# Optimization experiments

Hardware: AMD Instinct MI355X
Metric: run time of the kernel (lower is better)

The kernel has to match this reference:

```python
import jax, jax.numpy as jnp
import numpy as np

EPS = 1e-5  # torch LayerNorm default

def _layer_norm(v, w, b):
    mu = jnp.mean(v, axis=-1, keepdims=True)
    var = jnp.mean(jnp.square(v - mu), axis=-1, keepdims=True)
    return (v - mu) * jax.lax.rsqrt(var + EPS) * w + b

def _gru_layer(x, h0, w_ih, b_ih, w_hh, b_hh, ln_w, ln_b):
    # x: [B,T,in], h0: [B,H]
    H = h0.shape[-1]
    # precompute input gates for whole sequence: [B,T,3H]
    x_gates = jnp.einsum('bti,gi->btg', x, w_ih) + b_ih

    def step(h, xg_t):
        hg = jnp.einsum('bh,gh->bg', h, w_hh) + b_hh
        x_r, x_z, x_n = jnp.split(xg_t, 3, axis=-1)
        h_r, h_z, h_n = jnp.split(hg, 3, axis=-1)
        r = jax.nn.sigmoid(_layer_norm(x_r + h_r, ln_w[0], ln_b[0]))
        z = jax.nn.sigmoid(_layer_norm(x_z + h_z, ln_w[1], ln_b[1]))
        n = jnp.tanh(_layer_norm(x_n + r * h_n, ln_w[2], ln_b[2]))
        h_new = (1 - z) * n + z * h
        return h_new, h_new

    h_final, ys = jax.lax.scan(step, h0, jnp.swapaxes(x_gates, 0, 1))
    return jnp.swapaxes(ys, 0, 1), h_final  # [B,T,H], [B,H]

def setup_inputs() -> dict:
    key = jax.random.key(0)
    ks = jax.random.split(key, 4)
    B, T, D, H, L = 64, 512, 768, 768, 2
    G = 3 * H
    x = jax.random.normal(ks[0], (B, T, D), dtype=jnp.float32)
    h_0 = jnp.zeros((L, B, H), dtype=jnp.float32)
    # scaled gaussian stands in for orthogonal init
    w_ih = jax.random.normal(ks[1], (L, G, D), dtype=jnp.float32) / np.sqrt(D)
    w_hh = jax.random.normal(ks[2], (L, G, H), dtype=jnp.float32) / np.sqrt(H)
    b_ih = jnp.zeros((L, G), dtype=jnp.float32)
    b_hh = jnp.zeros((L, G), dtype=jnp.float32)
    ln_w = jnp.ones((L, 3, H), dtype=jnp.float32)
    ln_b = jnp.zeros((L, 3, H), dtype=jnp.float32)
    return {"x": x, "h_0": h_0, "w_ih": w_ih, "b_ih": b_ih,
            "w_hh": w_hh, "b_hh": b_hh, "ln_w": ln_w, "ln_b": ln_b}

def reference(x, h_0, w_ih, b_ih, w_hh, b_hh, ln_w, ln_b):
    num_layers = h_0.shape[0]
    layer_output = x
    x_residual = x  # input_size == hidden_size -> identity residual
    finals = []
    for i in range(num_layers):
        seq, h_fin = _gru_layer(layer_output, h_0[i], w_ih[i], b_ih[i],
                                w_hh[i], b_hh[i], ln_w[i], ln_b[i])
        if i == 0:
            seq = seq + x_residual
        else:
            seq = seq + layer_output
        layer_output = seq  # dropout=0.0, eval mode -> no-op
        finals.append(h_fin)
    h_final_stack = jnp.stack(finals, axis=0)
    return layer_output, h_final_stack
```

## Files before the change

### kernel.cpp

```cpp
#include <hip/hip_runtime.h>

typedef short bf16x8 __attribute__((ext_vector_type(8)));
typedef float f32x4 __attribute__((ext_vector_type(4)));

__device__ __forceinline__ unsigned pack2bf(float a, float b) {
  union { float f; unsigned u; } x, y;
  x.f = a; y.f = b;
  unsigned ra = (x.u + 0x7FFFu + ((x.u >> 16) & 1u)) >> 16;
  unsigned rb = (y.u + 0x7FFFu + ((y.u >> 16) & 1u)) & 0xFFFF0000u;
  return ra | rb;
}
__device__ __forceinline__ unsigned short bfu(float f) {
  union { float f; unsigned u; } v; v.f = f;
  return (unsigned short)((v.u + 0x7FFFu + ((v.u >> 16) & 1u)) >> 16);
}
__device__ __forceinline__ float sigf(float x) { return 1.f / (1.f + __expf(-x)); }

#define KB 64
#define LDSP 72

__global__ __launch_bounds__(256) void gemm_bt(
    const float* __restrict__ A0, size_t a_bstride,
    const float* __restrict__ W,
    const float* __restrict__ bias,
    float* __restrict__ out, size_t o_bstride,
    int Mvalid)
{
  __shared__ unsigned short As[64][LDSP];
  __shared__ unsigned short Bs[64][LDSP];
  const int tid = threadIdx.x;
  const int g0 = blockIdx.x * 64;
  const float* Ab = A0 + (size_t)blockIdx.y * a_bstride;
  float* outb = out + (size_t)blockIdx.y * o_bstride;

  const int srow = tid >> 2;
  const int scol = (tid & 3) << 4;
  const int wv = tid >> 6;
  const int lane = tid & 63;
  const int wr = wv >> 1, wc = wv & 1;
  const int lrow = lane & 15;
  const int lk = (lane >> 4) << 3;

  f32x4 acc[2][2];
#pragma unroll
  for (int i = 0; i < 2; ++i)
#pragma unroll
    for (int j = 0; j < 2; ++j)
      acc[i][j] = (f32x4){0.f, 0.f, 0.f, 0.f};

  const float* Aptr = Ab + (size_t)srow * 768 + scol;
  const float* Bptr = W + ((size_t)(g0 + srow)) * 768 + scol;
  const bool aval = srow < Mvalid;

  for (int k0 = 0; k0 < 768; k0 += KB) {
    uint4 ua0, ua1, ub0, ub1;
    if (aval) {
      const float4* qa = (const float4*)(Aptr + k0);
      float4 f0 = qa[0], f1 = qa[1], f2 = qa[2], f3 = qa[3];
      ua0 = make_uint4(pack2bf(f0.x, f0.y), pack2bf(f0.z, f0.w),
                       pack2bf(f1.x, f1.y), pack2bf(f1.z, f1.w));
      ua1 = make_uint4(pack2bf(f2.x, f2.y), pack2bf(f2.z, f2.w),
                       pack2bf(f3.x, f3.y), pack2bf(f3.z, f3.w));
    } else {
      ua0 = make_uint4(0u, 0u, 0u, 0u);
      ua1 = ua0;
    }
    {
      const float4* qb = (const float4*)(Bptr + k0);
      float4 f0 = qb[0], f1 = qb[1], f2 = qb[2], f3 = qb[3];
      ub0 = make_uint4(pack2bf(f0.x, f0.y), pack2bf(f0.z, f0.w),
                       pack2bf(f1.x, f1.y), pack2bf(f1.z, f1.w));
      ub1 = make_uint4(pack2bf(f2.x, f2.y), pack2bf(f2.z, f2.w),
                       pack2bf(f3.x, f3.y), pack2bf(f3.z, f3.w));
    }
    __syncthreads();
    *(uint4*)&As[srow][scol] = ua0;
    *(uint4*)&As[srow][scol + 8] = ua1;
    *(uint4*)&Bs[srow][scol] = ub0;
    *(uint4*)&Bs[srow][scol + 8] = ub1;
    __syncthreads();
#pragma unroll
    for (int kh = 0; kh < 2; ++kh) {
      bf16x8 a0 = *(const bf16x8*)&As[32 * wr + lrow][32 * kh + lk];
      bf16x8 a1 = *(const bf16x8*)&As[32 * wr + 16 + lrow][32 * kh + lk];
      bf16x8 b0 = *(const bf16x8*)&Bs[32 * wc + lrow][32 * kh + lk];
      bf16x8 b1 = *(const bf16x8*)&Bs[32 * wc + 16 + lrow][32 * kh + lk];
      acc[0][0] = __builtin_amdgcn_mfma_f32_16x16x32_bf16(a0, b0, acc[0][0], 0, 0, 0);
      acc[0][1] = __builtin_amdgcn_mfma_f32_16x16x32_bf16(a0, b1, acc[0][1], 0, 0, 0);
      acc[1][0] = __builtin_amdgcn_mfma_f32_16x16x32_bf16(a1, b0, acc[1][0], 0, 0, 0);
      acc[1][1] = __builtin_amdgcn_mfma_f32_16x16x32_bf16(a1, b1, acc[1][1], 0, 0, 0);
    }
  }

  const int lgrp = lane >> 4;
#pragma unroll
  for (int fr = 0; fr < 2; ++fr)
#pragma unroll
    for (int fc = 0; fc < 2; ++fc)
#pragma unroll
      for (int j = 0; j < 4; ++j) {
        int m = 32 * wr + 16 * fr + lgrp * 4 + j;
        int n = 32 * wc + 16 * fc + lrow;
        if (m < Mvalid)
          outb[(size_t)m * 2304 + g0 + n] = acc[fr][fc][j] + bias[g0 + n];
      }
}

#define NWG 72
#define EPS 1e-5f
#define INV768 (1.0f / 768.0f)
#define SLOT 24576u

__device__ __forceinline__ void bar_arrive(unsigned* c) {
  __syncthreads();
  if (threadIdx.x == 0)
    __hip_atomic_fetch_add(c + (blockIdx.x & 7) * 32, 1u,
                           __ATOMIC_RELAXED, __HIP_MEMORY_SCOPE_AGENT);
}
__device__ __forceinline__ void bar_wait(unsigned* c, unsigned tgt) {
  if (threadIdx.x == 0) {
    for (;;) {
      unsigned s = 0;
#pragma unroll
      for (int i = 0; i < 8; ++i)
        s += __hip_atomic_load(c + i * 32, __ATOMIC_RELAXED, __HIP_MEMORY_SCOPE_AGENT);
      if (s >= tgt) break;
      __builtin_amdgcn_s_sleep(1);
    }
  }
  __syncthreads();
}

template <int N>
__device__ __forceinline__ void blk_reduce(float* v, float* lds) {
#pragma unroll
  for (int k = 0; k < N; ++k) {
    float x = v[k];
#pragma unroll
    for (int off = 1; off < 64; off <<= 1) x += __shfl_xor(x, off);
    v[k] = x;
  }
  const int wv = threadIdx.x >> 6;
  const int lane = threadIdx.x & 63;
  if (lane == 0) {
#pragma unroll
    for (int k = 0; k < N; ++k) lds[wv * N + k] = v[k];
  }
  __syncthreads();
#pragma unroll
  for (int k = 0; k < N; ++k)
    v[k] = lds[k] + lds[N + k] + lds[2 * N + k] + lds[3 * N + k];
  __syncthreads();
}

#define WAITV(n) do { asm volatile("s_waitcnt vmcnt(" #n ")" ::: "memory"); \
                      __builtin_amdgcn_sched_barrier(0); } while (0)

#define LD24(buf, base) \
  { _Pragma("unroll") for (int kk_ = 0; kk_ < 24; ++kk_) { \
      const unsigned* p_ = (base) + (size_t)kk_ * 1024u; \
      asm volatile("global_load_dwordx4 %0, %1, off sc0 sc1" : "=v"(buf[kk_]) : "v"(p_)); } }

#define WRRING(ring, t, val) \
  { unsigned* rp_ = (ring) + (unsigned)(((t) & 3)) * SLOT; \
    _Pragma("unroll") for (int p_ = 0; p_ < 3; ++p_) { \
      int i_ = tid + (p_ << 8); \
      float other_ = __shfl_xor(val[p_], 1); \
      if ((tid & 1) == 0) { \
        unsigned pk_ = pack2bf(val[p_], other_); \
        __hip_atomic_store(rp_ + (i_ >> 3) * 256 + b * 4 + ((i_ >> 1) & 3), pk_, \
                           __ATOMIC_RELAXED, __HIP_MEMORY_SCOPE_AGENT); } } }

__global__ __launch_bounds__(256, 1) void gru_super(
    const float* __restrict__ Whh1, const float* __restrict__ bhh1,
    const float* __restrict__ Wih2, const float* __restrict__ bih2,
    const float* __restrict__ Whh2, const float* __restrict__ bhh2,
    const float* __restrict__ lnw, const float* __restrict__ lnb,
    const float* __restrict__ x,
    const float* __restrict__ xg1,
    int t0, int TC,
    const float* __restrict__ h0,
    float* __restrict__ hstate,
    unsigned* __restrict__ h1ring, unsigned* __restrict__ s1ring,
    unsigned* __restrict__ h2ring,
    float* __restrict__ hg1, float* __restrict__ xg2, float* __restrict__ hg2,
    unsigned* __restrict__ bar,
    float* __restrict__ seq,
    float* __restrict__ hfin,
    int firstflag, int lastflag)
{
  __shared__ unsigned short Wl[96][776];
  __shared__ float bl96[96];
  __shared__ float redl[32];

  unsigned* barA = bar;
  unsigned* barB = bar + 512;

  const int wg = blockIdx.x;
  const int tid = threadIdx.x;
  const int lane = tid & 63;
  const int w = tid >> 6;
  const int la = lane & 15;
  const int kb = lane >> 4;
  const int arow = 16 * w + la;
  const int mcls = wg / 24;
  const int g0w = (wg % 24) * 96;
  const unsigned abase = (unsigned)((kb * 64 + arow) << 2);

  {
    const float* Wsrc = (mcls == 0) ? Whh1 : (mcls == 1) ? Wih2 : Whh2;
    const float* bsrc = (mcls == 0) ? bhh1 : (mcls == 1) ? bih2 : bhh2;
    for (int r = 0; r < 96; ++r) {
      const float* src = Wsrc + (size_t)(g0w + r) * 768;
      for (int c = tid; c < 768; c += 256) Wl[r][c] = bfu(src[c]);
    }
    if (tid < 96) bl96[tid] = bsrc[g0w + tid];
  }
  float* dst = (mcls == 0) ? hg1 : (mcls == 1) ? xg2 : hg2;

  const int b = wg;
  float hreg1[3] = {0.f,0.f,0.f}, hreg2[3] = {0.f,0.f,0.f};
  float h1prev[3] = {0.f,0.f,0.f}, xprev[3] = {0.f,0.f,0.f}, xcur[3] = {0.f,0.f,0.f};
  float lw1[9], lb1[9], lw2[9], lb2[9];
  if (wg < 64) {
#pragma unroll
    for (int g = 0; g < 3; ++g)
#pragma unroll
      for (int p = 0; p < 3; ++p) {
        int idx = g * 3 + p, gi = g * 768 + tid + (p << 8);
        lw1[idx] = lnw[gi];          lb1[idx] = lnb[gi];
        lw2[idx] = lnw[2304 + gi];   lb2[idx] = lnb[2304 + gi];
      }
#pragma unroll
    for (int p = 0; p < 3; ++p) {
      int i = tid + (p << 8);
      hreg1[p] = firstflag ? h0[(size_t)b * 768 + i] : hstate[(size_t)b * 768 + i];
      hreg2[p] = firstflag ? h0[49152 + (size_t)b * 768 + i] : hstate[49152 + (size_t)b * 768 + i];
      h1prev[p] = hreg1[p];
    }
    if (firstflag) {
      WRRING(h1ring, 3, hreg1);
      WRRING(h2ring, 3, hreg2);
    }
  }
  bar_arrive(barB);
  bar_wait(barB, NWG);

  for (int s = 0; s <= TC; ++s) {
    const int t1 = t0 + s;
    const bool doL1 = (s < TC);
    const bool doL2 = (s >= 1);
    const bool active = (mcls == 0) ? doL1 : doL2;

    if (active) {
      const unsigned* rbase =
          (mcls == 0) ? (h1ring + (unsigned)((t1 - 1) & 3) * SLOT)
        : (mcls == 1) ? (s1ring + (unsigned)((t1 - 1) & 3) * SLOT)
                      : (h2ring + (unsigned)((t1 - 2) & 3) * SLOT);
      const unsigned* hb = rbase + abase;
      f32x4 acc[6];
#pragma unroll
      for (int r = 0; r < 6; ++r) acc[r] = (f32x4){0.f, 0.f, 0.f, 0.f};
      bf16x8 buf[24];
      LD24(buf, hb);
      WAITV(0);
#pragma unroll
      for (int kk = 0; kk < 24; ++kk) {
#pragma unroll
        for (int r = 0; r < 6; ++r) {
          bf16x8 wv = *(const bf16x8*)&Wl[16 * r + la][kk * 32 + kb * 8];
          acc[r] = __builtin_amdgcn_mfma_f32_16x16x32_bf16(buf[kk], wv, acc[r], 0, 0, 0);
        }
      }
#pragma unroll
      for (int r = 0; r < 6; ++r)
#pragma unroll
        for (int j = 0; j < 4; ++j) {
          int bb = 16 * w + kb * 4 + j;
          __hip_atomic_store(dst + (size_t)bb * 2304 + g0w + 16 * r + la,
                             acc[r][j] + bl96[16 * r + la],
                             __ATOMIC_RELAXED, __HIP_MEMORY_SCOPE_AGENT);
        }
    }

    if (wg < 64 && doL1) {
#pragma unroll
      for (int p = 0; p < 3; ++p)
        xcur[p] = x[((size_t)b * 512 + t1) * 768 + tid + (p << 8)];
    }

    bar_arrive(barA);
    bar_wait(barA, (unsigned)(s + 1) * NWG);

    if (wg < 64) {
      const int ttc = doL1 ? s : (TC - 1);
      float g1v[9], g2v[9], g3v[9], x1v[9];
      {
        const float* xg1b = xg1 + ((size_t)b * TC + ttc) * 2304;
        const float* p1 = hg1 + (size_t)b * 2304;
        const float* p2 = xg2 + (size_t)b * 2304;
        const float* p3 = hg2 + (size_t)b * 2304;
#pragma unroll
        for (int p = 0; p < 9; ++p) {
          x1v[p] = xg1b[tid + p * 256];
          const float* q1 = p1 + tid + p * 256;
          const float* q2 = p2 + tid + p * 256;
          const float* q3 = p3 + tid + p * 256;
          asm volatile("global_load_dword %0, %1, off sc0 sc1" : "=v"(g1v[p]) : "v"(q1));
          asm volatile("global_load_dword %0, %1, off sc0 sc1" : "=v"(g2v[p]) : "v"(q2));
          asm volatile("global_load_dword %0, %1, off sc0 sc1" : "=v"(g3v[p]) : "v"(q3));
        }
      }
      WAITV(0);

      float s11[3], s21[3], s12[3], s22[3];
      float v8[8] = {0,0,0,0,0,0,0,0};
#pragma unroll
      for (int p = 0; p < 3; ++p) {
        s11[p] = g1v[p] + x1v[p];
        s21[p] = g1v[3 + p] + x1v[3 + p];
        s12[p] = g2v[p] + g3v[p];
        s22[p] = g2v[3 + p] + g3v[3 + p];
        v8[0] += s11[p]; v8[1] += s11[p] * s11[p];
        v8[2] += s21[p]; v8[3] += s21[p] * s21[p];
        v8[4] += s12[p]; v8[5] += s12[p] * s12[p];
        v8[6] += s22[p]; v8[7] += s22[p] * s22[p];
      }
      blk_reduce<8>(v8, redl);
      float mu11 = v8[0] * INV768, rs11 = rsqrtf(v8[1] * INV768 - mu11 * mu11 + EPS);
      float mu21 = v8[2] * INV768, rs21 = rsqrtf(v8[3] * INV768 - mu21 * mu21 + EPS);
      float mu12 = v8[4] * INV768, rs12 = rsqrtf(v8[5] * INV768 - mu12 * mu12 + EPS);
      float mu22 = v8[6] * INV768, rs22 = rsqrtf(v8[7] * INV768 - mu22 * mu22 + EPS);

      float z1[3], m1[3], z2[3], m2[3];
      float v4[4] = {0,0,0,0};
#pragma unroll
      for (int p = 0; p < 3; ++p) {
        float r1 = sigf((s11[p] - mu11) * rs11 * lw1[p] + lb1[p]);
        z1[p]    = sigf((s21[p] - mu21) * rs21 * lw1[3 + p] + lb1[3 + p]);
        m1[p] = x1v[6 + p] + r1 * g1v[6 + p];
        float r2 = sigf((s12[p] - mu12) * rs12 * lw2[p] + lb2[p]);
        z2[p]    = sigf((s22[p] - mu22) * rs22 * lw2[3 + p] + lb2[3 + p]);
        m2[p] = g2v[6 + p] + r2 * g3v[6 + p];
        v4[0] += m1[p]; v4[1] += m1[p] * m1[p];
        v4[2] += m2[p]; v4[3] += m2[p] * m2[p];
      }
      blk_reduce<4>(v4, redl);
      float mum1 = v4[0] * INV768, rsm1 = rsqrtf(v4[1] * INV768 - mum1 * mum1 + EPS);
      float mum2 = v4[2] * INV768, rsm2 = rsqrtf(v4[3] * INV768 - mum2 * mum2 + EPS);

      float h1new[3], s1new[3], h2new[3];
#pragma unroll
      for (int p = 0; p < 3; ++p) {
        float n1 = tanhf((m1[p] - mum1) * rsm1 * lw1[6 + p] + lb1[6 + p]);
        h1new[p] = (1.f - z1[p]) * n1 + z1[p] * hreg1[p];
        s1new[p] = h1new[p] + xcur[p];
        float n2 = tanhf((m2[p] - mum2) * rsm2 * lw2[6 + p] + lb2[6 + p]);
        h2new[p] = (1.f - z2[p]) * n2 + z2[p] * hreg2[p];
      }
      if (doL2) {
        const int t2 = t1 - 1;
#pragma unroll
        for (int p = 0; p < 3; ++p) {
          int i = tid + (p << 8);
          hreg2[p] = h2new[p];
          seq[((size_t)b * 512 + t2) * 768 + i] = h2new[p] + h1prev[p] + xprev[p];
        }
        WRRING(h2ring, t1 - 1, h2new);
      }
      if (doL1) {
#pragma unroll
        for (int p = 0; p < 3; ++p) {
          hreg1[p] = h1new[p];
          h1prev[p] = h1new[p];
          xprev[p] = xcur[p];
        }
        WRRING(h1ring, t1, h1new);
        WRRING(s1ring, t1, s1new);
      }
    }
    bar_arrive(barB);
    bar_wait(barB, (unsigned)(s + 2) * NWG);
  }

  if (wg < 64) {
#pragma unroll
    for (int p = 0; p < 3; ++p) {
      int i = tid + (p << 8);
      hstate[(size_t)b * 768 + i] = hreg1[p];
      hstate[49152 + (size_t)b * 768 + i] = hreg2[p];
      if (lastflag) {
        hfin[(size_t)b * 768 + i] = hreg1[p];
        hfin[49152 + (size_t)b * 768 + i] = hreg2[p];
      }
    }
  }
}

extern "C" void kernel_launch(void* const* d_in, const int* in_sizes, int n_in,
                              void* d_out, int out_size, void* d_ws, size_t ws_size,
                              hipStream_t stream) {
  const float* x    = (const float*)d_in[0];
  const float* h0   = (const float*)d_in[1];
  const float* w_ih = (const float*)d_in[2];
  const float* b_ih = (const float*)d_in[3];
  const float* w_hh = (const float*)d_in[4];
  const float* b_hh = (const float*)d_in[5];
  const float* lnw  = (const float*)d_in[6];
  const float* lnb  = (const float*)d_in[7];
  float* out = (float*)d_out;

  const int B = 64, T = 512, H = 768, G = 2304;

  const size_t BAR = 65536;
  const size_t RING = 4u * SLOT * 4u;
  const size_t HGB = (size_t)B * G * 4;
  int CHUNK = 64;
  for (;;) {
    size_t need = BAR + 3 * RING + 3 * HGB + 2 * (size_t)B * H * 4
                + (size_t)B * CHUNK * G * 4;
    if (need <= ws_size || CHUNK == 8) break;
    CHUNK >>= 1;
  }

  char* wp = (char*)d_ws;
  unsigned* barctr = (unsigned*)wp;            wp += BAR;
  unsigned* h1ring = (unsigned*)wp;            wp += RING;
  unsigned* s1ring = (unsigned*)wp;            wp += RING;
  unsigned* h2ring = (unsigned*)wp;            wp += RING;
  float* hg1 = (float*)wp;                     wp += HGB;
  float* xg2 = (float*)wp;                     wp += HGB;
  float* hg2 = (float*)wp;                     wp += HGB;
  float* hstate = (float*)wp;                  wp += 2 * (size_t)B * H * 4;
  float* xg1 = (float*)wp;

  hipMemsetAsync(barctr, 0, BAR, stream);

  float* seq  = out;
  float* hfin = out + (size_t)B * T * H;
  const int NCH = T / CHUNK;

  const float* Wih1 = w_ih;
  const float* Wih2 = w_ih + (size_t)G * H;
  const float* Whh1 = w_hh;
  const float* Whh2 = w_hh + (size_t)G * H;

  for (int c = 0; c < NCH; ++c) {
    int t0 = c * CHUNK;
    gemm_bt<<<dim3(G / 64, B), 256, 0, stream>>>(
        x + (size_t)t0 * H, (size_t)T * H, Wih1, b_ih,
        xg1, (size_t)CHUNK * G, CHUNK);
    gru_super<<<NWG, 256, 0, stream>>>(
        Whh1, b_hh, Wih2, b_ih + G, Whh2, b_hh + G,
        lnw, lnb, x, xg1, t0, CHUNK,
        h0, hstate, h1ring, s1ring, h2ring,
        hg1, xg2, hg2,
        barctr + (size_t)c * 1024,
        seq, hfin,
        (c == 0) ? 1 : 0, (c == NCH - 1) ? 1 : 0);
  }
}
```

Measured before the change: 7.532 ms.

## Split GRU persistent kernel into producer matmul and consumer gate workgroups

The persistent recurrent kernel now uses 72 producer workgroups that only do the hidden-state matmuls and 64 separate consumer workgroups that do the LayerNorm/gate math. A symmetric full barrier per step is replaced by one-directional producer/consumer counters, so each side waits only on the other. Consumers prefetch xg1 and x before waiting and defer the seq store until after signalling. The chunk size doubles to 128 with a z-dimension added to the input GEMM to cover the extra rows. This is meant to cut barrier latency and overlap the two phases, at the cost of more resident workgroups (136) and a larger xg1 workspace.

```diff
diff --git a/kernel.cpp b/kernel.cpp
--- a/kernel.cpp
+++ b/kernel.cpp
@@ -30,8 +30,9 @@
   __shared__ unsigned short Bs[64][LDSP];
   const int tid = threadIdx.x;
   const int g0 = blockIdx.x * 64;
-  const float* Ab = A0 + (size_t)blockIdx.y * a_bstride;
-  float* outb = out + (size_t)blockIdx.y * o_bstride;
+  const int mlo = blockIdx.z * 64;
+  const float* Ab = A0 + (size_t)blockIdx.y * a_bstride + (size_t)mlo * 768;
+  float* outb = out + (size_t)blockIdx.y * o_bstride + (size_t)mlo * 2304;
 
   const int srow = tid >> 2;
   const int scol = (tid & 3) << 4;
@@ -50,7 +51,7 @@
 
   const float* Aptr = Ab + (size_t)srow * 768 + scol;
   const float* Bptr = W + ((size_t)(g0 + srow)) * 768 + scol;
-  const bool aval = srow < Mvalid;
+  const bool aval = (mlo + srow) < Mvalid;
 
   for (int k0 = 0; k0 < 768; k0 += KB) {
     uint4 ua0, ua1, ub0, ub1;
@@ -101,12 +102,14 @@
       for (int j = 0; j < 4; ++j) {
         int m = 32 * wr + 16 * fr + lgrp * 4 + j;
         int n = 32 * wc + 16 * fc + lrow;
-        if (m < Mvalid)
+        if (mlo + m < Mvalid)
           outb[(size_t)m * 2304 + g0 + n] = acc[fr][fc][j] + bias[g0 + n];
       }
 }
 
-#define NWG 72
+#define NWGP 72
+#define NWGC 64
+#define NWGT 136
 #define EPS 1e-5f
 #define INV768 (1.0f / 768.0f)
 #define SLOT 24576u
@@ -203,196 +206,205 @@
   const int la = lane & 15;
   const int kb = lane >> 4;
   const int arow = 16 * w + la;
-  const int mcls = wg / 24;
-  const int g0w = (wg % 24) * 96;
-  const unsigned abase = (unsigned)((kb * 64 + arow) << 2);
-
-  {
-    const float* Wsrc = (mcls == 0) ? Whh1 : (mcls == 1) ? Wih2 : Whh2;
-    const float* bsrc = (mcls == 0) ? bhh1 : (mcls == 1) ? bih2 : bhh2;
-    for (int r = 0; r < 96; ++r) {
-      const float* src = Wsrc + (size_t)(g0w + r) * 768;
-      for (int c = tid; c < 768; c += 256) Wl[r][c] = bfu(src[c]);
-    }
-    if (tid < 96) bl96[tid] = bsrc[g0w + tid];
-  }
-  float* dst = (mcls == 0) ? hg1 : (mcls == 1) ? xg2 : hg2;
-
-  const int b = wg;
-  float hreg1[3] = {0.f,0.f,0.f}, hreg2[3] = {0.f,0.f,0.f};
-  float h1prev[3] = {0.f,0.f,0.f}, xprev[3] = {0.f,0.f,0.f}, xcur[3] = {0.f,0.f,0.f};
+
+  if (wg < NWGP) {
+    const int mcls = wg / 24;
+    const int g0w = (wg % 24) * 96;
+    const unsigned abase = (unsigned)((kb * 64 + arow) << 2);
+    {
+      const float* Wsrc = (mcls == 0) ? Whh1 : (mcls == 1) ? Wih2 : Whh2;
+      const float* bsrc = (mcls == 0) ? bhh1 : (mcls == 1) ? bih2 : bhh2;
+      for (int r = 0; r < 96; ++r) {
+        const float* src = Wsrc + (size_t)(g0w + r) * 768;
+        for (int c = tid; c < 768; c += 256) Wl[r][c] = bfu(src[c]);
+      }
+      if (tid < 96) bl96[tid] = bsrc[g0w + tid];
+    }
+    float* dst = (mcls == 0) ? hg1 : (mcls == 1) ? xg2 : hg2;
+
+    for (int s = 0; s <= TC; ++s) {
+      const int t1 = t0 + s;
+      const bool active = (mcls == 0) ? (s < TC) : (s >= 1);
+      bar_wait(barB, 64u * (unsigned)(s + 1));
+      if (active) {
+        const unsigned* rbase =
+            (mcls == 0) ? (h1ring + (unsigned)((t1 - 1) & 3) * SLOT)
+          : (mcls == 1) ? (s1ring + (unsigned)((t1 - 1) & 3) * SLOT)
+                        : (h2ring + (unsigned)((t1 - 2) & 3) * SLOT);
+        const unsigned* hb = rbase + abase;
+        f32x4 acc[6];
+#pragma unroll
+        for (int r = 0; r < 6; ++r) acc[r] = (f32x4){0.f, 0.f, 0.f, 0.f};
+        bf16x8 buf[24];
+        LD24(buf, hb);
+        WAITV(0);
+#pragma unroll
+        for (int kk = 0; kk < 24; ++kk) {
+#pragma unroll
+          for (int r = 0; r < 6; ++r) {
+            bf16x8 wv2 = *(const bf16x8*)&Wl[16 * r + la][kk * 32 + kb * 8];
+            acc[r] = __builtin_amdgcn_mfma_f32_16x16x32_bf16(buf[kk], wv2, acc[r], 0, 0, 0);
+          }
+        }
+#pragma unroll
+        for (int r = 0; r < 6; ++r)
+#pragma unroll
+          for (int j = 0; j < 4; ++j) {
+            int bb = 16 * w + kb * 4 + j;
+            __hip_atomic_store(dst + (size_t)bb * 2304 + g0w + 16 * r + la,
+                               acc[r][j] + bl96[16 * r + la],
+                               __ATOMIC_RELAXED, __HIP_MEMORY_SCOPE_AGENT);
+          }
+      }
+      bar_arrive(barA);
+    }
+    return;
+  }
+
+  const int b = wg - NWGP;
+  float hreg1[3], hreg2[3];
+  float h1prev[3], xprev[3] = {0.f, 0.f, 0.f}, xcur[3] = {0.f, 0.f, 0.f};
   float lw1[9], lb1[9], lw2[9], lb2[9];
-  if (wg < 64) {
-#pragma unroll
-    for (int g = 0; g < 3; ++g)
-#pragma unroll
-      for (int p = 0; p < 3; ++p) {
-        int idx = g * 3 + p, gi = g * 768 + tid + (p << 8);
-        lw1[idx] = lnw[gi];          lb1[idx] = lnb[gi];
-        lw2[idx] = lnw[2304 + gi];   lb2[idx] = lnb[2304 + gi];
-      }
+#pragma unroll
+  for (int g = 0; g < 3; ++g)
 #pragma unroll
     for (int p = 0; p < 3; ++p) {
-      int i = tid + (p << 8);
-      hreg1[p] = firstflag ? h0[(size_t)b * 768 + i] : hstate[(size_t)b * 768 + i];
-      hreg2[p] = firstflag ? h0[49152 + (size_t)b * 768 + i] : hstate[49152 + (size_t)b * 768 + i];
-      h1prev[p] = hreg1[p];
-    }
-    if (firstflag) {
-      WRRING(h1ring, 3, hreg1);
-      WRRING(h2ring, 3, hreg2);
-    }
+      int idx = g * 3 + p, gi = g * 768 + tid + (p << 8);
+      lw1[idx] = lnw[gi];          lb1[idx] = lnb[gi];
+      lw2[idx] = lnw[2304 + gi];   lb2[idx] = lnb[2304 + gi];
+    }
+#pragma unroll
+  for (int p = 0; p < 3; ++p) {
+    int i = tid + (p << 8);
+    hreg1[p] = firstflag ? h0[(size_t)b * 768 + i] : hstate[(size_t)b * 768 + i];
+    hreg2[p] = firstflag ? h0[49152 + (size_t)b * 768 + i] : hstate[49152 + (size_t)b * 768 + i];
+    h1prev[p] = hreg1[p];
+  }
+  if (firstflag) {
+    WRRING(h1ring, 3, hreg1);
+    WRRING(h2ring, 3, hreg2);
   }
   bar_arrive(barB);
-  bar_wait(barB, NWG);
 
   for (int s = 0; s <= TC; ++s) {
     const int t1 = t0 + s;
     const bool doL1 = (s < TC);
     const bool doL2 = (s >= 1);
-    const bool active = (mcls == 0) ? doL1 : doL2;
-
-    if (active) {
-      const unsigned* rbase =
-          (mcls == 0) ? (h1ring + (unsigned)((t1 - 1) & 3) * SLOT)
-        : (mcls == 1) ? (s1ring + (unsigned)((t1 - 1) & 3) * SLOT)
-                      : (h2ring + (unsigned)((t1 - 2) & 3) * SLOT);
-      const unsigned* hb = rbase + abase;
-      f32x4 acc[6];
-#pragma unroll
-      for (int r = 0; r < 6; ++r) acc[r] = (f32x4){0.f, 0.f, 0.f, 0.f};
-      bf16x8 buf[24];
-      LD24(buf, hb);
-      WAITV(0);
-#pragma unroll
-      for (int kk = 0; kk < 24; ++kk) {
-#pragma unroll
-        for (int r = 0; r < 6; ++r) {
-          bf16x8 wv = *(const bf16x8*)&Wl[16 * r + la][kk * 32 + kb * 8];
-          acc[r] = __builtin_amdgcn_mfma_f32_16x16x32_bf16(buf[kk], wv, acc[r], 0, 0, 0);
-        }
-      }
-#pragma unroll
-      for (int r = 0; r < 6; ++r)
-#pragma unroll
-        for (int j = 0; j < 4; ++j) {
-          int bb = 16 * w + kb * 4 + j;
-          __hip_atomic_store(dst + (size_t)bb * 2304 + g0w + 16 * r + la,
-                             acc[r][j] + bl96[16 * r + la],
-                             __ATOMIC_RELAXED, __HIP_MEMORY_SCOPE_AGENT);
-        }
-    }
-
-    if (wg < 64 && doL1) {
+
+    const int ttc = doL1 ? s : (TC - 1);
+    float x1v[9];
+    {
+      const float* xg1b = xg1 + ((size_t)b * TC + ttc) * 2304;
+#pragma unroll
+      for (int p = 0; p < 9; ++p) x1v[p] = xg1b[tid + p * 256];
+    }
+    if (doL1) {
 #pragma unroll
       for (int p = 0; p < 3; ++p)
         xcur[p] = x[((size_t)b * 512 + t1) * 768 + tid + (p << 8)];
     }
 
-    bar_arrive(barA);
-    bar_wait(barA, (unsigned)(s + 1) * NWG);
-
-    if (wg < 64) {
-      const int ttc = doL1 ? s : (TC - 1);
-      float g1v[9], g2v[9], g3v[9], x1v[9];
-      {
-        const float* xg1b = xg1 + ((size_t)b * TC + ttc) * 2304;
-        const float* p1 = hg1 + (size_t)b * 2304;
-        const float* p2 = xg2 + (size_t)b * 2304;
-        const float* p3 = hg2 + (size_t)b * 2304;
-#pragma unroll
-        for (int p = 0; p < 9; ++p) {
-          x1v[p] = xg1b[tid + p * 256];
-          const float* q1 = p1 + tid + p * 256;
-          const float* q2 = p2 + tid + p * 256;
-          const float* q3 = p3 + tid + p * 256;
-          asm volatile("global_load_dword %0, %1, off sc0 sc1" : "=v"(g1v[p]) : "v"(q1));
-          asm volatile("global_load_dword %0, %1, off sc0 sc1" : "=v"(g2v[p]) : "v"(q2));
-          asm volatile("global_load_dword %0, %1, off sc0 sc1" : "=v"(g3v[p]) : "v"(q3));
-        }
-      }
-      WAITV(0);
-
-      float s11[3], s21[3], s12[3], s22[3];
-      float v8[8] = {0,0,0,0,0,0,0,0};
+    bar_wait(barA, 72u * (unsigned)(s + 1));
+
+    float g1v[9], g2v[9], g3v[9];
+    {
+      const float* p1 = hg1 + (size_t)b * 2304;
+      const float* p2 = xg2 + (size_t)b * 2304;
+      const float* p3 = hg2 + (size_t)b * 2304;
+#pragma unroll
+      for (int p = 0; p < 9; ++p) {
+        const float* q1 = p1 + tid + p * 256;
+        const float* q2 = p2 + tid + p * 256;
+        const float* q3 = p3 + tid + p * 256;
+        asm volatile("global_load_dword %0, %1, off sc0 sc1" : "=v"(g1v[p]) : "v"(q1));
+        asm volatile("global_load_dword %0, %1, off sc0 sc1" : "=v"(g2v[p]) : "v"(q2));
+        asm volatile("global_load_dword %0, %1, off sc0 sc1" : "=v"(g3v[p]) : "v"(q3));
+      }
+    }
+    WAITV(0);
+
+    float s11[3], s21[3], s12[3], s22[3];
+    float v8[8] = {0,0,0,0,0,0,0,0};
+#pragma unroll
+    for (int p = 0; p < 3; ++p) {
+      s11[p] = g1v[p] + x1v[p];
+      s21[p] = g1v[3 + p] + x1v[3 + p];
+      s12[p] = g2v[p] + g3v[p];
+      s22[p] = g2v[3 + p] + g3v[3 + p];
+      v8[0] += s11[p]; v8[1] += s11[p] * s11[p];
+      v8[2] += s21[p]; v8[3] += s21[p] * s21[p];
+      v8[4] += s12[p]; v8[5] += s12[p] * s12[p];
+      v8[6] += s22[p]; v8[7] += s22[p] * s22[p];
+    }
+    blk_reduce<8>(v8, redl);
+    float mu11 = v8[0] * INV768, rs11 = rsqrtf(v8[1] * INV768 - mu11 * mu11 + EPS);
+    float mu21 = v8[2] * INV768, rs21 = rsqrtf(v8[3] * INV768 - mu21 * mu21 + EPS);
+    float mu12 = v8[4] * INV768, rs12 = rsqrtf(v8[5] * INV768 - mu12 * mu12 + EPS);
+    float mu22 = v8[6] * INV768, rs22 = rsqrtf(v8[7] * INV768 - mu22 * mu22 + EPS);
+
+    float z1[3], m1[3], z2[3], m2[3];
+    float v4[4] = {0,0,0,0};
+#pragma unroll
+    for (int p = 0; p < 3; ++p) {
+      float r1 = sigf((s11[p] - mu11) * rs11 * lw1[p] + lb1[p]);
+      z1[p]    = sigf((s21[p] - mu21) * rs21 * lw1[3 + p] + lb1[3 + p]);
+      m1[p] = x1v[6 + p] + r1 * g1v[6 + p];
+      float r2 = sigf((s12[p] - mu12) * rs12 * lw2[p] + lb2[p]);
+      z2[p]    = sigf((s22[p] - mu22) * rs22 * lw2[3 + p] + lb2[3 + p]);
+      m2[p] = g2v[6 + p] + r2 * g3v[6 + p];
+      v4[0] += m1[p]; v4[1] += m1[p] * m1[p];
+      v4[2] += m2[p]; v4[3] += m2[p] * m2[p];
+    }
+    blk_reduce<4>(v4, redl);
+    float mum1 = v4[0] * INV768, rsm1 = rsqrtf(v4[1] * INV768 - mum1 * mum1 + EPS);
+    float mum2 = v4[2] * INV768, rsm2 = rsqrtf(v4[3] * INV768 - mum2 * mum2 + EPS);
+
+    float h1new[3], s1new[3], h2new[3], seqv[3];
+#pragma unroll
+    for (int p = 0; p < 3; ++p) {
+      float n1 = tanhf((m1[p] - mum1) * rsm1 * lw1[6 + p] + lb1[6 + p]);
+      h1new[p] = (1.f - z1[p]) * n1 + z1[p] * hreg1[p];
+      s1new[p] = h1new[p] + xcur[p];
+      float n2 = tanhf((m2[p] - mum2) * rsm2 * lw2[6 + p] + lb2[6 + p]);
+      h2new[p] = (1.f - z2[p]) * n2 + z2[p] * hreg2[p];
+    }
+    if (doL2) {
 #pragma unroll
       for (int p = 0; p < 3; ++p) {
-        s11[p] = g1v[p] + x1v[p];
-        s21[p] = g1v[3 + p] + x1v[3 + p];
-        s12[p] = g2v[p] + g3v[p];
-        s22[p] = g2v[3 + p] + g3v[3 + p];
-        v8[0] += s11[p]; v8[1] += s11[p] * s11[p];
-        v8[2] += s21[p]; v8[3] += s21[p] * s21[p];
-        v8[4] += s12[p]; v8[5] += s12[p] * s12[p];
-        v8[6] += s22[p]; v8[7] += s22[p] * s22[p];
-      }
-      blk_reduce<8>(v8, redl);
-      float mu11 = v8[0] * INV768, rs11 = rsqrtf(v8[1] * INV768 - mu11 * mu11 + EPS);
-      float mu21 = v8[2] * INV768, rs21 = rsqrtf(v8[3] * INV768 - mu21 * mu21 + EPS);
-      float mu12 = v8[4] * INV768, rs12 = rsqrtf(v8[5] * INV768 - mu12 * mu12 + EPS);
-      float mu22 = v8[6] * INV768, rs22 = rsqrtf(v8[7] * INV768 - mu22 * mu22 + EPS);
-
-      float z1[3], m1[3], z2[3], m2[3];
-      float v4[4] = {0,0,0,0};
+        hreg2[p] = h2new[p];
+        seqv[p] = h2new[p] + h1prev[p] + xprev[p];
+      }
+      WRRING(h2ring, t1 - 1, h2new);
+    }
+    if (doL1) {
 #pragma unroll
       for (int p = 0; p < 3; ++p) {
-        float r1 = sigf((s11[p] - mu11) * rs11 * lw1[p] + lb1[p]);
-        z1[p]    = sigf((s21[p] - mu21) * rs21 * lw1[3 + p] + lb1[3 + p]);
-        m1[p] = x1v[6 + p] + r1 * g1v[6 + p];
-        float r2 = sigf((s12[p] - mu12) * rs12 * lw2[p] + lb2[p]);
-        z2[p]    = sigf((s22[p] - mu22) * rs22 * lw2[3 + p] + lb2[3 + p]);
-        m2[p] = g2v[6 + p] + r2 * g3v[6 + p];
-        v4[0] += m1[p]; v4[1] += m1[p] * m1[p];
-        v4[2] += m2[p]; v4[3] += m2[p] * m2[p];
-      }
-      blk_reduce<4>(v4, redl);
-      float mum1 = v4[0] * INV768, rsm1 = rsqrtf(v4[1] * INV768 - mum1 * mum1 + EPS);
-      float mum2 = v4[2] * INV768, rsm2 = rsqrtf(v4[3] * INV768 - mum2 * mum2 + EPS);
-
-      float h1new[3], s1new[3], h2new[3];
+        hreg1[p] = h1new[p];
+        h1prev[p] = h1new[p];
+        xprev[p] = xcur[p];
+      }
+      WRRING(h1ring, t1, h1new);
+      WRRING(s1ring, t1, s1new);
+    }
+    bar_arrive(barB);
+    if (doL2) {
+      const int t2 = t1 - 1;
 #pragma unroll
       for (int p = 0; p < 3; ++p) {
-        float n1 = tanhf((m1[p] - mum1) * rsm1 * lw1[6 + p] + lb1[6 + p]);
-        h1new[p] = (1.f - z1[p]) * n1 + z1[p] * hreg1[p];
-        s1new[p] = h1new[p] + xcur[p];
-        float n2 = tanhf((m2[p] - mum2) * rsm2 * lw2[6 + p] + lb2[6 + p]);
-        h2new[p] = (1.f - z2[p]) * n2 + z2[p] * hreg2[p];
-      }
-      if (doL2) {
-        const int t2 = t1 - 1;
-#pragma unroll
-        for (int p = 0; p < 3; ++p) {
-          int i = tid + (p << 8);
-          hreg2[p] = h2new[p];
-          seq[((size_t)b * 512 + t2) * 768 + i] = h2new[p] + h1prev[p] + xprev[p];
-        }
-        WRRING(h2ring, t1 - 1, h2new);
-      }
-      if (doL1) {
-#pragma unroll
-        for (int p = 0; p < 3; ++p) {
-          hreg1[p] = h1new[p];
-          h1prev[p] = h1new[p];
-          xprev[p] = xcur[p];
-        }
-        WRRING(h1ring, t1, h1new);
-        WRRING(s1ring, t1, s1new);
-      }
-    }
-    bar_arrive(barB);
-    bar_wait(barB, (unsigned)(s + 2) * NWG);
-  }
-
-  if (wg < 64) {
-#pragma unroll
-    for (int p = 0; p < 3; ++p) {
-      int i = tid + (p << 8);
-      hstate[(size_t)b * 768 + i] = hreg1[p];
-      hstate[49152 + (size_t)b * 768 + i] = hreg2[p];
-      if (lastflag) {
-        hfin[(size_t)b * 768 + i] = hreg1[p];
-        hfin[49152 + (size_t)b * 768 + i] = hreg2[p];
-      }
+        int i = tid + (p << 8);
+        seq[((size_t)b * 512 + t2) * 768 + i] = seqv[p];
+      }
+    }
+  }
+
+#pragma unroll
+  for (int p = 0; p < 3; ++p) {
+    int i = tid + (p << 8);
+    hstate[(size_t)b * 768 + i] = hreg1[p];
+    hstate[49152 + (size_t)b * 768 + i] = hreg2[p];
+    if (lastflag) {
+      hfin[(size_t)b * 768 + i] = hreg1[p];
+      hfin[49152 + (size_t)b * 768 + i] = hreg2[p];
     }
   }
 }
@@ -415,7 +427,7 @@
   const size_t BAR = 65536;
   const size_t RING = 4u * SLOT * 4u;
   const size_t HGB = (size_t)B * G * 4;
-  int CHUNK = 64;
+  int CHUNK = 128;
   for (;;) {
     size_t need = BAR + 3 * RING + 3 * HGB + 2 * (size_t)B * H * 4
                 + (size_t)B * CHUNK * G * 4;
@@ -447,10 +459,10 @@
 
   for (int c = 0; c < NCH; ++c) {
     int t0 = c * CHUNK;
-    gemm_bt<<<dim3(G / 64, B), 256, 0, stream>>>(
+    gemm_bt<<<dim3(G / 64, B, CHUNK / 64), 256, 0, stream>>>(
         x + (size_t)t0 * H, (size_t)T * H, Wih1, b_ih,
         xg1, (size_t)CHUNK * G, CHUNK);
-    gru_super<<<NWG, 256, 0, stream>>>(
+    gru_super<<<NWGT, 256, 0, stream>>>(
         Whh1, b_hh, Wih2, b_ih + G, Whh2, b_hh + G,
         lnw, lnb, x, xg1, t0, CHUNK,
         h0, hstate, h1ring, s1ring, h2ring,
```

Result: faster. 6.639 ms (-11.9%).
